# Kernel optimization log

Measured on AMD Instinct MI355X. Metric: run time of the kernel, lower is better.

Reference implementation:

```python
import jax, jax.numpy as jnp
import numpy as np

ALG = 8  # octonion algebra dimension
_TRIPLES = [(1,2,3),(1,4,5),(1,7,6),(2,4,6),(2,5,7),(3,4,7),(3,6,5)]

def _oct_table():
    # Cayley multiplication table: e_i * e_j = S[i,j] * e_{K[i,j]}
    K = np.zeros((8,8), np.int64); S = np.zeros((8,8), np.int64)
    K[0,:] = np.arange(8); S[0,:] = 1
    K[:,0] = np.arange(8); S[:,0] = 1
    for i in range(1,8):
        K[i,i] = 0; S[i,i] = -1
    for (a,b,c) in _TRIPLES:
        for x,y,z in ((a,b,c),(b,c,a),(c,a,b)):
            K[x,y] = z; S[x,y] = 1
            K[y,x] = z; S[y,x] = -1
    return K, S

_K, _S = _oct_table()

def _ternary(w):
    # BitNet-style absmean ternary quantization (STE is irrelevant for fwd)
    scale = jnp.mean(jnp.abs(w)) + 1e-8
    wq = jnp.clip(jnp.round(w / scale), -1.0, 1.0) * scale
    return w + jax.lax.stop_gradient(wq - w)

def _oct_big(w):
    # w: [8, din8, dout8] -> structured dense [8*din8, 8*dout8]
    # out_k = sum_{i,j: e_i e_j = s e_k} s * x_i @ W_j  (64 static blocks)
    din8, dout8 = w.shape[1], w.shape[2]
    big = jnp.zeros((8, din8, 8, dout8), w.dtype)
    for i in range(8):
        for j in range(8):
            big = big.at[i, :, int(_K[i, j]), :].set(float(_S[i, j]) * w[j])
    return big.reshape(8 * din8, 8 * dout8)

def _oct_linear(x, w):
    return x @ _oct_big(_ternary(w))

def setup_inputs() -> dict:
    key = jax.random.key(0)
    k1, k2, k3, k4 = jax.random.split(key, 4)
    B, T, D = 8, 4096, 768
    H = 2048  # int(2*4*768/3) rounded up to multiple of 8
    d8, h8 = D // ALG, H // ALG
    x = jax.random.normal(k1, (B, T, D), dtype=jnp.float32)
    w_gate = 0.02 * jax.random.normal(k2, (ALG, d8, h8), dtype=jnp.float32)
    w_up   = 0.02 * jax.random.normal(k3, (ALG, d8, h8), dtype=jnp.float32)
    w_down = 0.02 * jax.random.normal(k4, (ALG, h8, d8), dtype=jnp.float32)
    return {"x": x, "w_gate": w_gate, "w_up": w_up, "w_down": w_down}

def reference(x, w_gate, w_up, w_down):
    gate = _oct_linear(x, w_gate)          # [B,T,H]
    up   = _oct_linear(x, w_up)            # [B,T,H]
    h    = jax.nn.silu(gate) * up          # SwiGLU gate
    return _oct_linear(h, w_down)          # [B,T,D]
```

## Files before the change

### kernel.cpp

```cpp
#include <hip/hip_runtime.h>
#include <hip/hip_bf16.h>

typedef unsigned short u16;
typedef unsigned int u32;
typedef float f32x4 __attribute__((ext_vector_type(4)));
typedef __bf16 bf16x8 __attribute__((ext_vector_type(8)));

#define AS1 __attribute__((address_space(1)))
#define AS3 __attribute__((address_space(3)))

#define MTOT 32768
#define DK   768
#define HN   2048

__constant__ signed char J_TAB[64] = {
  0,1,2,3,4,5,6,7,
  1,0,3,2,5,4,7,6,
  2,3,0,1,6,7,4,5,
  3,2,1,0,7,6,5,4,
  4,5,6,7,0,1,2,3,
  5,4,7,6,1,0,3,2,
  6,7,4,5,2,3,0,1,
  7,6,5,4,3,2,1,0};
__constant__ signed char S_TAB[64] = {
   1, 1, 1, 1, 1, 1, 1, 1,
  -1, 1,-1, 1,-1, 1, 1,-1,
  -1, 1, 1,-1,-1,-1, 1, 1,
  -1,-1, 1, 1,-1, 1,-1, 1,
  -1, 1, 1, 1, 1,-1,-1,-1,
  -1,-1, 1,-1, 1, 1, 1,-1,
  -1,-1,-1, 1, 1,-1, 1, 1,
  -1, 1,-1,-1, 1, 1,-1, 1};

__device__ __forceinline__ u16 f2bf(float f) {
  u32 x = __float_as_uint(f);
  x += 0x7fffu + ((x >> 16) & 1u);
  return (u16)(x >> 16);
}

__device__ __forceinline__ void gload_lds16(const void* g, void* l) {
  __builtin_amdgcn_global_load_lds((AS1 void*)(g), (AS3 void*)(l), 16, 0, 0);
}

#define VMW(N) do { __builtin_amdgcn_sched_barrier(0); \
  asm volatile("s_waitcnt vmcnt(" #N ")" ::: "memory"); \
  __builtin_amdgcn_sched_barrier(0); } while (0)
#define BAR() do { __builtin_amdgcn_sched_barrier(0); \
  __builtin_amdgcn_s_barrier(); \
  __builtin_amdgcn_sched_barrier(0); } while (0)

template <int LDK>
__device__ __forceinline__ void stage_half(const u16* __restrict__ src,
                                           u16* lds, int tid) {
#pragma unroll
  for (int f0 = 0; f0 < 1024; f0 += 512) {
    int flat = f0 + tid;
    int row = flat >> 3;
    int c = (flat & 7) ^ (row & 7);
    gload_lds16(src + row * LDK + c * 8, lds + (f0 + (tid & ~63)) * 8);
  }
}

template <int ROWS, int LDK>
__device__ __forceinline__ void stage_tile(const u16* __restrict__ src,
                                           u16* lds, int tid) {
#pragma unroll
  for (int f0 = 0; f0 < ROWS * 8; f0 += 256) {
    int flat = f0 + tid;
    int row = flat >> 3;
    int c = (flat & 7) ^ (row & 7);
    gload_lds16(src + row * LDK + c * 8, lds + (f0 + (tid & 192)) * 8);
  }
}

template <int LDK, bool SA, bool SB, int VM>
__device__ __forceinline__ void ktile4(
    const u16* lAp, const u16* lBp, u16* lAn, u16* lBn,
    const u16* __restrict__ aStage, const u16* __restrict__ bStage,
    int tid, int arow, int brow, int c0, int c1, f32x4 (&acc)[8][4]) {
  bf16x8 a0[4], a1[4], a2[4], a3[4], b0[4], b1[4];
#pragma unroll
  for (int mi = 0; mi < 4; ++mi)
    a0[mi] = *(const bf16x8*)(lAp + (arow + mi * 16) * 64 + c0);
#pragma unroll
  for (int ni = 0; ni < 4; ++ni)
    b0[ni] = *(const bf16x8*)(lBp + (brow + ni * 16) * 64 + c0);
#pragma unroll
  for (int mi = 0; mi < 4; ++mi)
    a1[mi] = *(const bf16x8*)(lAp + (arow + mi * 16) * 64 + c1);
#pragma unroll
  for (int ni = 0; ni < 4; ++ni)
    b1[ni] = *(const bf16x8*)(lBp + (brow + ni * 16) * 64 + c1);
  if constexpr (SA) stage_half<LDK>(aStage, lAn, tid);
  BAR();
  __builtin_amdgcn_s_setprio(1);
#pragma unroll
  for (int mi = 0; mi < 4; ++mi)
#pragma unroll
    for (int ni = 0; ni < 4; ++ni)
      acc[mi][ni] = __builtin_amdgcn_mfma_f32_16x16x32_bf16(
          a0[mi], b0[ni], acc[mi][ni], 0, 0, 0);
  __builtin_amdgcn_s_setprio(0);
  BAR();
#pragma unroll
  for (int mi = 0; mi < 4; ++mi)
    a2[mi] = *(const bf16x8*)(lAp + (arow + 64 + mi * 16) * 64 + c0);
  if constexpr (SA) stage_half<LDK>(aStage + 128 * LDK, lAn + 128 * 64, tid);
  BAR();
  __builtin_amdgcn_s_setprio(1);
#pragma unroll
  for (int mi = 0; mi < 4; ++mi)
#pragma unroll
    for (int ni = 0; ni < 4; ++ni)
      acc[mi][ni] = __builtin_amdgcn_mfma_f32_16x16x32_bf16(
          a1[mi], b1[ni], acc[mi][ni], 0, 0, 0);
  __builtin_amdgcn_s_setprio(0);
  BAR();
#pragma unroll
  for (int mi = 0; mi < 4; ++mi)
    a3[mi] = *(const bf16x8*)(lAp + (arow + 64 + mi * 16) * 64 + c1);
  if constexpr (SB) stage_half<LDK>(bStage, lBn, tid);
  BAR();
  __builtin_amdgcn_s_setprio(1);
#pragma unroll
  for (int mi = 0; mi < 4; ++mi)
#pragma unroll
    for (int ni = 0; ni < 4; ++ni)
      acc[4 + mi][ni] = __builtin_amdgcn_mfma_f32_16x16x32_bf16(
          a2[mi], b0[ni], acc[4 + mi][ni], 0, 0, 0);
  __builtin_amdgcn_s_setprio(0);
  BAR();
  if constexpr (SB) stage_half<LDK>(bStage + 128 * LDK, lBn + 128 * 64, tid);
  if constexpr (VM == 4) VMW(4);
  else if constexpr (VM == 0) VMW(0);
  BAR();
  __builtin_amdgcn_s_setprio(1);
#pragma unroll
  for (int mi = 0; mi < 4; ++mi)
#pragma unroll
    for (int ni = 0; ni < 4; ++ni)
      acc[4 + mi][ni] = __builtin_amdgcn_mfma_f32_16x16x32_bf16(
          a3[mi], b1[ni], acc[4 + mi][ni], 0, 0, 0);
  __builtin_amdgcn_s_setprio(0);
  BAR();
}

template <int NK, int LDK>
__device__ __forceinline__ void gemm_core(const u16* __restrict__ aSrc,
                                          const u16* __restrict__ bSrc, int tid,
                                          u16* lA0, u16* lA1, u16* lB0, u16* lB1,
                                          f32x4 (&acc)[8][4]) {
  const int lane = tid & 63;
  const int wave = tid >> 6;
  const int wm = wave >> 2, wn = wave & 3;
  const int l15 = lane & 15, quad = (lane >> 4) & 3;
  const int arow = wm * 128 + l15;
  const int brow = wn * 64 + l15;
  const int c0 = (quad ^ (l15 & 7)) * 8;
  const int c1 = ((quad + 4) ^ (l15 & 7)) * 8;

  stage_half<LDK>(aSrc, lA0, tid);
  stage_half<LDK>(aSrc + 128 * LDK, lA0 + 128 * 64, tid);
  stage_half<LDK>(bSrc, lB0, tid);
  stage_half<LDK>(bSrc + 128 * LDK, lB0 + 128 * 64, tid);
  stage_half<LDK>(bSrc + 64, lB1, tid);
  stage_half<LDK>(bSrc + 64 + 128 * LDK, lB1 + 128 * 64, tid);
  VMW(4);
  BAR();

#pragma unroll 1
  for (int i = 0; i < NK / 2 - 1; ++i) {
    ktile4<LDK, true, true, 4>(lA0, lB0, lA1, lB0,
                               aSrc + (2 * i + 1) * 64, bSrc + (2 * i + 2) * 64,
                               tid, arow, brow, c0, c1, acc);
    ktile4<LDK, true, true, 4>(lA1, lB1, lA0, lB1,
                               aSrc + (2 * i + 2) * 64, bSrc + (2 * i + 3) * 64,
                               tid, arow, brow, c0, c1, acc);
  }
  ktile4<LDK, true, false, 0>(lA0, lB0, lA1, lB0,
                              aSrc + (NK - 1) * 64, nullptr,
                              tid, arow, brow, c0, c1, acc);
  ktile4<LDK, false, false, -1>(lA1, lB1, lA0, lB1, nullptr, nullptr,
                                tid, arow, brow, c0, c1, acc);
}

__global__ void scales1_kernel(const float* __restrict__ w0,
                               const float* __restrict__ w1,
                               const float* __restrict__ w2,
                               float* __restrict__ partials) {
  __shared__ float red[256];
  const int t = blockIdx.x / 192;
  const int chunk = blockIdx.x % 192;
  const float* w = (t == 0) ? w0 : (t == 1) ? w1 : w2;
  const float4* w4 = (const float4*)(w + chunk * 1024);
  float4 v = w4[threadIdx.x];
  red[threadIdx.x] = fabsf(v.x) + fabsf(v.y) + fabsf(v.z) + fabsf(v.w);
  __syncthreads();
  for (int off = 128; off; off >>= 1) {
    if (threadIdx.x < off) red[threadIdx.x] += red[threadIdx.x + off];
    __syncthreads();
  }
  if (threadIdx.x == 0) partials[blockIdx.x] = red[0];
}

__global__ void scales2_kernel(const float* __restrict__ partials,
                               float* __restrict__ scales) {
  __shared__ float red[256];
  float s = (threadIdx.x < 192) ? partials[blockIdx.x * 192 + threadIdx.x] : 0.f;
  red[threadIdx.x] = s;
  __syncthreads();
  for (int off = 128; off; off >>= 1) {
    if (threadIdx.x < off) red[threadIdx.x] += red[threadIdx.x + off];
    __syncthreads();
  }
  if (threadIdx.x == 0) scales[blockIdx.x] = red[0] / 196608.f + 1e-8f;
}

__global__ void build_big_kernel(const float* __restrict__ w,
                                 const float* __restrict__ scales, int sidx,
                                 int A, int B, int ilv, u16* __restrict__ dst) {
  int idx = blockIdx.x * 256 + threadIdx.x;
  int K8 = 8 * A;
  int n = idx / K8;
  int k = idx - n * K8;
  int i = k / A, a = k - i * A;
  int c = n / B, b = n - c * B;
  float scale = scales[sidx];
  int j = J_TAB[i * 8 + c];
  float q = rintf(w[(j * A + a) * B + b] / scale);
  q = fminf(1.f, fmaxf(-1.f, q));
  int nd = (ilv >= 0) ? (((n & ~15) << 1) | (ilv << 4) | (n & 15)) : n;
  int kd = (ilv == -2) ? ((k & ~31) | ((k & 15) << 1) | ((k >> 4) & 1)) : k;
  dst[nd * K8 + kd] = f2bf(q * (float)S_TAB[i * 8 + c]);
}

__global__ void cvt_x_kernel(const float* __restrict__ x, u16* __restrict__ xb) {
  int gid = blockIdx.x * 256 + threadIdx.x;
  const float4* x4 = (const float4*)x;
  float4 v0 = x4[gid * 2], v1 = x4[gid * 2 + 1];
  uint4 o;
  o.x = (u32)f2bf(v0.x) | ((u32)f2bf(v0.y) << 16);
  o.y = (u32)f2bf(v0.z) | ((u32)f2bf(v0.w) << 16);
  o.z = (u32)f2bf(v1.x) | ((u32)f2bf(v1.y) << 16);
  o.w = (u32)f2bf(v1.z) | ((u32)f2bf(v1.w) << 16);
  ((uint4*)xb)[gid] = o;
}

__global__ __launch_bounds__(512, 2) void gemm1_kernel(
    const u16* __restrict__ xb, const u16* __restrict__ wgu,
    const float* __restrict__ scales, u16* __restrict__ h) {
  __shared__ __align__(16) u16 lA0[256 * 64], lA1[256 * 64];
  __shared__ __align__(16) u16 lB0[256 * 64], lB1[256 * 64];
  const int tid = threadIdx.x;
  const int logical = (blockIdx.x & 7) * 256 + (blockIdx.x >> 3);
  const int bn = logical & 15;
  const int bm = logical >> 4;
  const int m0 = bm * 256, n0 = bn * 256;

  f32x4 acc[8][4] = {};
  gemm_core<12, DK>(xb + (size_t)m0 * DK, wgu + (size_t)n0 * DK, tid,
                    lA0, lA1, lB0, lB1, acc);

  const int lane = tid & 63, wave = tid >> 6;
  const int wm = wave >> 2, wn = wave & 3;
  const int l15 = lane & 15, quad = lane >> 4;
  const float sg = scales[0], su = scales[1];
  const int a_ = bn * 4 + wn;
  u32* h32 = (u32*)h;
#pragma unroll
  for (int mi = 0; mi < 8; ++mi)
#pragma unroll
    for (int r = 0; r < 4; ++r) {
      int m = m0 + wm * 128 + mi * 16 + quad * 4 + r;
      float g0 = acc[mi][0][r] * sg, u0 = acc[mi][1][r] * su;
      float g1 = acc[mi][2][r] * sg, u1 = acc[mi][3][r] * su;
      float h0 = g0 / (1.f + __expf(-g0)) * u0;
      float h1 = g1 / (1.f + __expf(-g1)) * u1;
      h32[(size_t)m * (HN / 2) + a_ * 16 + l15] =
          (u32)f2bf(h0) | ((u32)f2bf(h1) << 16);
    }
}

__global__ __launch_bounds__(256, 2) void gemm2_kernel(
    const u16* __restrict__ h, const u16* __restrict__ wd,
    const float* __restrict__ scales, float* __restrict__ out) {
  __shared__ __align__(16) u16 lA[2][64 * 64];
  __shared__ __align__(16) u16 lB[2][256 * 64];
  const int tid = threadIdx.x;
  const int logical = (blockIdx.x & 7) * 192 + (blockIdx.x >> 3);
  const int bn = logical % 3;
  const int bm = logical / 3;
  const int m0 = bm * 64, n0 = bn * 256;
  const u16* aSrc = h + (size_t)m0 * HN;
  const u16* bSrc = wd + (size_t)n0 * HN;

  const int lane = tid & 63, wave = tid >> 6;
  const int l15 = lane & 15, quad = (lane >> 4) & 3;
  const int brow = wave * 64 + l15;
  const int c0 = (quad ^ (l15 & 7)) * 8;
  const int c1 = ((quad + 4) ^ (l15 & 7)) * 8;

  f32x4 acc[4][4] = {};

  stage_tile<64, HN>(aSrc, lA[0], tid);
  stage_tile<256, HN>(bSrc, lB[0], tid);

#pragma unroll 1
  for (int S = 0; S < HN / 64; ++S) {
    if (S < HN / 64 - 1) {
      stage_tile<64, HN>(aSrc + (S + 1) * 64, lA[(S + 1) & 1], tid);
      stage_tile<256, HN>(bSrc + (S + 1) * 64, lB[(S + 1) & 1], tid);
      VMW(10);
    } else {
      VMW(0);
    }
    BAR();
    const u16* la = lA[S & 1];
    const u16* lb = lB[S & 1];
    bf16x8 af[4][2], bf[4][2];
#pragma unroll
    for (int mi = 0; mi < 4; ++mi) {
      const u16* p = la + (l15 + mi * 16) * 64;
      af[mi][0] = *(const bf16x8*)(p + c0);
      af[mi][1] = *(const bf16x8*)(p + c1);
    }
#pragma unroll
    for (int ni = 0; ni < 4; ++ni) {
      const u16* p = lb + (brow + ni * 16) * 64;
      bf[ni][0] = *(const bf16x8*)(p + c0);
      bf[ni][1] = *(const bf16x8*)(p + c1);
    }
    __builtin_amdgcn_s_setprio(1);
#pragma unroll
    for (int k = 0; k < 2; ++k)
#pragma unroll
      for (int mi = 0; mi < 4; ++mi)
#pragma unroll
        for (int ni = 0; ni < 4; ++ni)
          acc[mi][ni] = __builtin_amdgcn_mfma_f32_16x16x32_bf16(
              af[mi][k], bf[ni][k], acc[mi][ni], 0, 0, 0);
    __builtin_amdgcn_s_setprio(0);
    BAR();
  }

  const float sd = scales[2];
#pragma unroll
  for (int mi = 0; mi < 4; ++mi)
#pragma unroll
    for (int ni = 0; ni < 4; ++ni) {
      const int n = n0 + wave * 64 + ni * 16 + l15;
#pragma unroll
      for (int r = 0; r < 4; ++r) {
        int m = m0 + mi * 16 + quad * 4 + r;
        out[(size_t)m * DK + n] = acc[mi][ni][r] * sd;
      }
    }
}

extern "C" void kernel_launch(void* const* d_in, const int* in_sizes, int n_in,
                              void* d_out, int out_size, void* d_ws, size_t ws_size,
                              hipStream_t stream) {
  const float* x      = (const float*)d_in[0];
  const float* w_gate = (const float*)d_in[1];
  const float* w_up   = (const float*)d_in[2];
  const float* w_down = (const float*)d_in[3];
  float* out = (float*)d_out;

  char* ws = (char*)d_ws;
  float* scales   = (float*)ws;
  float* partials = (float*)(ws + 256);
  u16* wgu = (u16*)(ws + 4096);
  u16* wd  = (u16*)(ws + 4096 + 6291456u);
  u16* xb  = (u16*)(ws + 4096 + 9437184u);
  u16* h   = (u16*)(ws + 4096 + 9437184u + 50331648u);

  scales1_kernel<<<576, 256, 0, stream>>>(w_gate, w_up, w_down, partials);
  scales2_kernel<<<3, 256, 0, stream>>>(partials, scales);
  build_big_kernel<<<6144, 256, 0, stream>>>(w_gate, scales, 0, 96, 256, 0, wgu);
  build_big_kernel<<<6144, 256, 0, stream>>>(w_up,   scales, 1, 96, 256, 1, wgu);
  build_big_kernel<<<6144, 256, 0, stream>>>(w_down, scales, 2, 256, 96, -2, wd);
  cvt_x_kernel<<<12288, 256, 0, stream>>>(x, xb);
  gemm1_kernel<<<2048, 512, 0, stream>>>(xb, wgu, scales, h);
  gemm2_kernel<<<1536, 256, 0, stream>>>(h, wd, scales, out);
}
```

Baseline: 572.2 us.

## Restructure down-projection GEMM: direct-register A loads and triple-buffered B k32 tiles

Gemm2 now keeps the activation operand A in registers, loaded straight from global memory one k-step ahead, instead of staging it through LDS. The weight operand B is staged in 32-wide k slices through a triple-buffered LDS ring with a new swizzle. The aim is to cut LDS traffic and LDS footprint and to overlap loads with MFMA work using one barrier per k-step. In exchange, the direct global A loads are less coalesced, and the VMW/BAR macros no longer carry sched_barriers, which changes the compiler's scheduling freedom in gemm2.

```diff
diff --git a/kernel.cpp b/kernel.cpp
--- a/kernel.cpp
+++ b/kernel.cpp
@@ -42,12 +42,14 @@
   __builtin_amdgcn_global_load_lds((AS1 void*)(g), (AS3 void*)(l), 16, 0, 0);
 }
 
-#define VMW(N) do { __builtin_amdgcn_sched_barrier(0); \
+#define PVMW(N) do { __builtin_amdgcn_sched_barrier(0); \
   asm volatile("s_waitcnt vmcnt(" #N ")" ::: "memory"); \
   __builtin_amdgcn_sched_barrier(0); } while (0)
-#define BAR() do { __builtin_amdgcn_sched_barrier(0); \
+#define PBAR() do { __builtin_amdgcn_sched_barrier(0); \
   __builtin_amdgcn_s_barrier(); \
   __builtin_amdgcn_sched_barrier(0); } while (0)
+#define VMW(N) asm volatile("s_waitcnt vmcnt(" #N ")" ::: "memory")
+#define BAR() __builtin_amdgcn_s_barrier()
 
 template <int LDK>
 __device__ __forceinline__ void stage_half(const u16* __restrict__ src,
@@ -58,18 +60,6 @@
     int row = flat >> 3;
     int c = (flat & 7) ^ (row & 7);
     gload_lds16(src + row * LDK + c * 8, lds + (f0 + (tid & ~63)) * 8);
-  }
-}
-
-template <int ROWS, int LDK>
-__device__ __forceinline__ void stage_tile(const u16* __restrict__ src,
-                                           u16* lds, int tid) {
-#pragma unroll
-  for (int f0 = 0; f0 < ROWS * 8; f0 += 256) {
-    int flat = f0 + tid;
-    int row = flat >> 3;
-    int c = (flat & 7) ^ (row & 7);
-    gload_lds16(src + row * LDK + c * 8, lds + (f0 + (tid & 192)) * 8);
   }
 }
 
@@ -92,7 +82,7 @@
   for (int ni = 0; ni < 4; ++ni)
     b1[ni] = *(const bf16x8*)(lBp + (brow + ni * 16) * 64 + c1);
   if constexpr (SA) stage_half<LDK>(aStage, lAn, tid);
-  BAR();
+  PBAR();
   __builtin_amdgcn_s_setprio(1);
 #pragma unroll
   for (int mi = 0; mi < 4; ++mi)
@@ -101,12 +91,12 @@
       acc[mi][ni] = __builtin_amdgcn_mfma_f32_16x16x32_bf16(
           a0[mi], b0[ni], acc[mi][ni], 0, 0, 0);
   __builtin_amdgcn_s_setprio(0);
-  BAR();
+  PBAR();
 #pragma unroll
   for (int mi = 0; mi < 4; ++mi)
     a2[mi] = *(const bf16x8*)(lAp + (arow + 64 + mi * 16) * 64 + c0);
   if constexpr (SA) stage_half<LDK>(aStage + 128 * LDK, lAn + 128 * 64, tid);
-  BAR();
+  PBAR();
   __builtin_amdgcn_s_setprio(1);
 #pragma unroll
   for (int mi = 0; mi < 4; ++mi)
@@ -115,12 +105,12 @@
       acc[mi][ni] = __builtin_amdgcn_mfma_f32_16x16x32_bf16(
           a1[mi], b1[ni], acc[mi][ni], 0, 0, 0);
   __builtin_amdgcn_s_setprio(0);
-  BAR();
+  PBAR();
 #pragma unroll
   for (int mi = 0; mi < 4; ++mi)
     a3[mi] = *(const bf16x8*)(lAp + (arow + 64 + mi * 16) * 64 + c1);
   if constexpr (SB) stage_half<LDK>(bStage, lBn, tid);
-  BAR();
+  PBAR();
   __builtin_amdgcn_s_setprio(1);
 #pragma unroll
   for (int mi = 0; mi < 4; ++mi)
@@ -129,11 +119,11 @@
       acc[4 + mi][ni] = __builtin_amdgcn_mfma_f32_16x16x32_bf16(
           a2[mi], b0[ni], acc[4 + mi][ni], 0, 0, 0);
   __builtin_amdgcn_s_setprio(0);
-  BAR();
+  PBAR();
   if constexpr (SB) stage_half<LDK>(bStage + 128 * LDK, lBn + 128 * 64, tid);
-  if constexpr (VM == 4) VMW(4);
-  else if constexpr (VM == 0) VMW(0);
-  BAR();
+  if constexpr (VM == 4) PVMW(4);
+  else if constexpr (VM == 0) PVMW(0);
+  PBAR();
   __builtin_amdgcn_s_setprio(1);
 #pragma unroll
   for (int mi = 0; mi < 4; ++mi)
@@ -142,7 +132,7 @@
       acc[4 + mi][ni] = __builtin_amdgcn_mfma_f32_16x16x32_bf16(
           a3[mi], b1[ni], acc[4 + mi][ni], 0, 0, 0);
   __builtin_amdgcn_s_setprio(0);
-  BAR();
+  PBAR();
 }
 
 template <int NK, int LDK>
@@ -165,8 +155,8 @@
   stage_half<LDK>(bSrc + 128 * LDK, lB0 + 128 * 64, tid);
   stage_half<LDK>(bSrc + 64, lB1, tid);
   stage_half<LDK>(bSrc + 64 + 128 * LDK, lB1 + 128 * 64, tid);
-  VMW(4);
-  BAR();
+  PVMW(4);
+  PBAR();
 
 #pragma unroll 1
   for (int i = 0; i < NK / 2 - 1; ++i) {
@@ -182,6 +172,50 @@
                               tid, arow, brow, c0, c1, acc);
   ktile4<LDK, false, false, -1>(lA1, lB1, lA0, lB1, nullptr, nullptr,
                                 tid, arow, brow, c0, c1, acc);
+}
+
+__device__ __forceinline__ int sw3(int r) { return (r ^ (r >> 2)) & 3; }
+
+__device__ __forceinline__ void stage_b32(const u16* __restrict__ src,
+                                          u16* lds, int tid) {
+#pragma unroll
+  for (int f0 = 0; f0 < 1024; f0 += 256) {
+    int flat = f0 + tid;
+    int row = flat >> 2;
+    int c = (flat & 3) ^ sw3(row);
+    gload_lds16(src + (size_t)row * HN + c * 8, lds + (f0 + (tid & ~63)) * 8);
+  }
+}
+
+template <bool STG, bool ANXT, int VM>
+__device__ __forceinline__ void ktile_g2(
+    const u16* lBread, u16* lBwrite,
+    const u16* __restrict__ bStage, const u16* __restrict__ aNxtSrc,
+    bf16x8 (&aCur)[4], bf16x8 (&aNxt)[4],
+    int tid, int brow, int quad, f32x4 (&acc)[4][4]) {
+  bf16x8 bf[4];
+#pragma unroll
+  for (int ni = 0; ni < 4; ++ni) {
+    int row = brow + ni * 16;
+    bf[ni] = *(const bf16x8*)(lBread + row * 32 + (quad ^ sw3(row)) * 8);
+  }
+  if constexpr (STG) stage_b32(bStage, lBwrite, tid);
+  if constexpr (ANXT) {
+#pragma unroll
+    for (int mi = 0; mi < 4; ++mi)
+      aNxt[mi] = *(const bf16x8*)(aNxtSrc + (size_t)mi * 16 * HN);
+  }
+  __builtin_amdgcn_s_setprio(1);
+#pragma unroll
+  for (int mi = 0; mi < 4; ++mi)
+#pragma unroll
+    for (int ni = 0; ni < 4; ++ni)
+      acc[mi][ni] = __builtin_amdgcn_mfma_f32_16x16x32_bf16(
+          aCur[mi], bf[ni], acc[mi][ni], 0, 0, 0);
+  __builtin_amdgcn_s_setprio(0);
+  if constexpr (VM == 8) VMW(8);
+  else if constexpr (VM == 0) VMW(0);
+  BAR();
 }
 
 __global__ void scales1_kernel(const float* __restrict__ w0,
@@ -284,64 +318,44 @@
 __global__ __launch_bounds__(256, 2) void gemm2_kernel(
     const u16* __restrict__ h, const u16* __restrict__ wd,
     const float* __restrict__ scales, float* __restrict__ out) {
-  __shared__ __align__(16) u16 lA[2][64 * 64];
-  __shared__ __align__(16) u16 lB[2][256 * 64];
+  __shared__ __align__(16) u16 lB[3][256 * 32];
   const int tid = threadIdx.x;
   const int logical = (blockIdx.x & 7) * 192 + (blockIdx.x >> 3);
   const int bn = logical % 3;
   const int bm = logical / 3;
   const int m0 = bm * 64, n0 = bn * 256;
-  const u16* aSrc = h + (size_t)m0 * HN;
-  const u16* bSrc = wd + (size_t)n0 * HN;
 
   const int lane = tid & 63, wave = tid >> 6;
   const int l15 = lane & 15, quad = (lane >> 4) & 3;
   const int brow = wave * 64 + l15;
-  const int c0 = (quad ^ (l15 & 7)) * 8;
-  const int c1 = ((quad + 4) ^ (l15 & 7)) * 8;
+  const u16* bSrc = wd + (size_t)n0 * HN;
+  const u16* aBase = h + (size_t)(m0 + l15) * HN + quad * 8;
 
   f32x4 acc[4][4] = {};
-
-  stage_tile<64, HN>(aSrc, lA[0], tid);
-  stage_tile<256, HN>(bSrc, lB[0], tid);
-
+  bf16x8 aA[4], aB[4];
+
+  stage_b32(bSrc, lB[0], tid);
+  stage_b32(bSrc + 32, lB[1], tid);
+#pragma unroll
+  for (int mi = 0; mi < 4; ++mi)
+    aA[mi] = *(const bf16x8*)(aBase + (size_t)mi * 16 * HN);
+  VMW(8);
+  BAR();
+
+  u16 *q0 = lB[0], *q1 = lB[1], *q2 = lB[2];
 #pragma unroll 1
-  for (int S = 0; S < HN / 64; ++S) {
-    if (S < HN / 64 - 1) {
-      stage_tile<64, HN>(aSrc + (S + 1) * 64, lA[(S + 1) & 1], tid);
-      stage_tile<256, HN>(bSrc + (S + 1) * 64, lB[(S + 1) & 1], tid);
-      VMW(10);
-    } else {
-      VMW(0);
-    }
-    BAR();
-    const u16* la = lA[S & 1];
-    const u16* lb = lB[S & 1];
-    bf16x8 af[4][2], bf[4][2];
-#pragma unroll
-    for (int mi = 0; mi < 4; ++mi) {
-      const u16* p = la + (l15 + mi * 16) * 64;
-      af[mi][0] = *(const bf16x8*)(p + c0);
-      af[mi][1] = *(const bf16x8*)(p + c1);
-    }
-#pragma unroll
-    for (int ni = 0; ni < 4; ++ni) {
-      const u16* p = lb + (brow + ni * 16) * 64;
-      bf[ni][0] = *(const bf16x8*)(p + c0);
-      bf[ni][1] = *(const bf16x8*)(p + c1);
-    }
-    __builtin_amdgcn_s_setprio(1);
-#pragma unroll
-    for (int k = 0; k < 2; ++k)
-#pragma unroll
-      for (int mi = 0; mi < 4; ++mi)
-#pragma unroll
-        for (int ni = 0; ni < 4; ++ni)
-          acc[mi][ni] = __builtin_amdgcn_mfma_f32_16x16x32_bf16(
-              af[mi][k], bf[ni][k], acc[mi][ni], 0, 0, 0);
-    __builtin_amdgcn_s_setprio(0);
-    BAR();
-  }
+  for (int it = 0; it < 31; ++it) {
+    const int T = 2 * it;
+    ktile_g2<true, true, 8>(q0, q2, bSrc + (T + 2) * 32,
+                            aBase + (T + 1) * 32, aA, aB, tid, brow, quad, acc);
+    ktile_g2<true, true, 8>(q1, q0, bSrc + (T + 3) * 32,
+                            aBase + (T + 2) * 32, aB, aA, tid, brow, quad, acc);
+    u16* t = q0; q0 = q2; q2 = q1; q1 = t;
+  }
+  ktile_g2<false, true, 8>(q0, nullptr, nullptr, aBase + 63 * 32,
+                           aA, aB, tid, brow, quad, acc);
+  ktile_g2<false, false, -1>(q1, nullptr, nullptr, nullptr,
+                             aB, aA, tid, brow, quad, acc);
 
   const float sd = scales[2];
 #pragma unroll
```

Result: slower. 675.0 us (+18.0%).
